# Optimization experiments

Measured on AMD Instinct MI355X. Metric: run time of the kernel, lower is better.

The kernel has to match this reference:

```python
import math
import jax, jax.numpy as jnp
import numpy as np

HIDDEN = 1024
HEADS = 8
HEAD = HIDDEN // HEADS  # 128
BATCH = 512
EPS = 1e-6
GN_EPS = 1e-5


def setup_inputs() -> dict:
    key = jax.random.key(0)
    ks = jax.random.split(key, 12)
    inp = {
        "q": jax.random.normal(ks[0], (BATCH, HIDDEN), jnp.float32),
        "k": jax.random.normal(ks[1], (BATCH, HIDDEN), jnp.float32),
        "v": jax.random.normal(ks[2], (BATCH, HIDDEN), jnp.float32),
        "cell_state": jax.random.normal(ks[3], (BATCH, HEADS, HEAD, HEAD), jnp.float32),
        "norm_state": jax.random.normal(ks[4], (BATCH, HEADS, HEAD), jnp.float32),
        "max_state": jax.random.normal(ks[5], (BATCH, HEADS), jnp.float32),
        # learned params
        "Wi": jax.random.normal(ks[6], (HEADS, 3 * HIDDEN), jnp.float32) / math.sqrt(3 * HIDDEN),
        "bi": jax.random.normal(ks[7], (HEADS,), jnp.float32) * 0.1,
        "Wf": jax.random.normal(ks[8], (HEADS, 3 * HIDDEN), jnp.float32) / math.sqrt(3 * HIDDEN),
        "bf": jax.random.normal(ks[9], (HEADS,), jnp.float32) * 0.1,
        "gn_gamma": jnp.ones((HIDDEN,), jnp.float32),
        "gn_beta": jnp.zeros((HIDDEN,), jnp.float32),
    }
    return inp


def reference(q, k, v, cell_state, norm_state, max_state, Wi, bi, Wf, bf, gn_gamma, gn_beta):
    B, H, D = q.shape[0], HEADS, HEAD
    qkv = jnp.concatenate([q, k, v], axis=-1)           # (B, 3*hidden)
    igate_preact = qkv @ Wi.T + bi                       # (B, H)
    fgate_preact = qkv @ Wf.T + bf                       # (B, H)

    qh = q.reshape(B, H, D)
    kh = k.reshape(B, H, D) * (1.0 / math.sqrt(D))
    vh = v.reshape(B, H, D)

    log_f = jax.nn.log_sigmoid(fgate_preact)
    max_new = jnp.maximum(igate_preact, max_state + log_f)
    i_gate = jnp.exp(igate_preact - max_new)             # (B, H)
    f_gate = jnp.exp(log_f + max_state - max_new)        # (B, H)

    # matrix state update: (B, H, D, D)
    cell_new = f_gate[:, :, None, None] * cell_state + \
               i_gate[:, :, None, None] * kh[:, :, :, None] * vh[:, :, None, :]
    norm_new = f_gate[:, :, None] * norm_state + i_gate[:, :, None] * kh

    numerator = jnp.einsum('bnh,bnhk->bnk', qh, cell_new)   # (B, H, D)
    qn_dot = jnp.einsum('bnh,bnh->bn', qh, norm_new)        # (B, H)
    denominator = jnp.maximum(jnp.abs(qn_dot), jnp.exp(-max_new)) + EPS
    out = numerator / denominator[:, :, None]               # (B, H, D)

    # GroupNorm: num_groups = H, per-group over D channels, per-channel affine
    mu = jnp.mean(out, axis=-1, keepdims=True)
    var = jnp.var(out, axis=-1, keepdims=True)
    out = (out - mu) / jnp.sqrt(var + GN_EPS)
    out = out.reshape(B, H * D) * gn_gamma + gn_beta

    return out, cell_new, norm_new, max_new
```

## Files before the change

### kernel.cpp

```cpp
#include <hip/hip_runtime.h>
#include <math.h>

#define HIDDEN 1024
#define HEADS 8
#define HEAD 128
#define BATCH 512
#define RSQRT_D 0.08838834764831845f

__global__ __launch_bounds__(256) void gates_kernel(
    const float* __restrict__ q, const float* __restrict__ k,
    const float* __restrict__ v, const float* __restrict__ max_state,
    const float* __restrict__ Wi, const float* __restrict__ bi,
    const float* __restrict__ Wf, const float* __restrict__ bf,
    float* __restrict__ ig_out, float* __restrict__ fg_out,
    float* __restrict__ expnm_out, float* __restrict__ maxnew_out)
{
    const int b = blockIdx.x;
    const int t = threadIdx.x;

    float acc_i[HEADS], acc_f[HEADS];
    #pragma unroll
    for (int h = 0; h < HEADS; ++h) { acc_i[h] = 0.f; acc_f[h] = 0.f; }

    const float* qr = q + b * HIDDEN;
    const float* kr = k + b * HIDDEN;
    const float* vr = v + b * HIDDEN;

    for (int j = t; j < 3 * HIDDEN; j += 256) {
        float x = (j < HIDDEN) ? qr[j]
                : (j < 2 * HIDDEN) ? kr[j - HIDDEN]
                : vr[j - 2 * HIDDEN];
        #pragma unroll
        for (int h = 0; h < HEADS; ++h) {
            acc_i[h] = fmaf(x, Wi[h * 3 * HIDDEN + j], acc_i[h]);
            acc_f[h] = fmaf(x, Wf[h * 3 * HIDDEN + j], acc_f[h]);
        }
    }

    #pragma unroll
    for (int h = 0; h < HEADS; ++h) {
        #pragma unroll
        for (int off = 32; off > 0; off >>= 1) {
            acc_i[h] += __shfl_down(acc_i[h], off, 64);
            acc_f[h] += __shfl_down(acc_f[h], off, 64);
        }
    }

    __shared__ float part[4][16];
    __shared__ float pre[16];
    const int wave = t >> 6, lane = t & 63;
    if (lane == 0) {
        #pragma unroll
        for (int h = 0; h < HEADS; ++h) {
            part[wave][h]     = acc_i[h];
            part[wave][8 + h] = acc_f[h];
        }
    }
    __syncthreads();
    if (t < 16) pre[t] = part[0][t] + part[1][t] + part[2][t] + part[3][t];
    __syncthreads();

    if (t < HEADS) {
        float igp = pre[t] + bi[t];
        float fgp = pre[8 + t] + bf[t];
        float lf = (fgp >= 0.f) ? -log1pf(expf(-fgp)) : (fgp - log1pf(expf(fgp)));
        float m_old = max_state[b * HEADS + t];
        float m_new = fmaxf(igp, m_old + lf);
        const int idx = b * HEADS + t;
        ig_out[idx]    = expf(igp - m_new);
        fg_out[idx]    = expf(lf + m_old - m_new);
        expnm_out[idx] = expf(-m_new);
        maxnew_out[idx] = m_new;
    }
}

__global__ __launch_bounds__(256) void mlstm_main(
    const float* __restrict__ q, const float* __restrict__ k,
    const float* __restrict__ v,
    const float* __restrict__ cell_state, const float* __restrict__ norm_state,
    const float* __restrict__ gn_gamma, const float* __restrict__ gn_beta,
    const float* __restrict__ ig, const float* __restrict__ fg,
    const float* __restrict__ expnm,
    float* __restrict__ out, float* __restrict__ cell_new,
    float* __restrict__ norm_new)
{
    const int bh = blockIdx.x;
    const int b = bh >> 3, h = bh & 7;
    const int t = threadIdx.x;
    const int tx = t & 31, ty = t >> 5;

    __shared__ __align__(16) float q_s[HEAD];
    __shared__ __align__(16) float ikh_s[HEAD];
    __shared__ float4 red[8][32];
    __shared__ float inv_denom_s;

    const float i_gate = ig[bh];
    const float f_gate = fg[bh];

    const float* qrow = q + b * HIDDEN + h * HEAD;
    const float* krow = k + b * HIDDEN + h * HEAD;
    const float* vrow = v + b * HIDDEN + h * HEAD;

    if (t < HEAD) {
        q_s[t]   = qrow[t];
        ikh_s[t] = i_gate * krow[t] * RSQRT_D;
    }
    __syncthreads();

    const float4* c_in  = (const float4*)(cell_state + (size_t)bh * HEAD * HEAD);
    float4*       c_out = (float4*)(cell_new   + (size_t)bh * HEAD * HEAD);

    const float4 v4 = ((const float4*)vrow)[tx];

    float4 num = make_float4(0.f, 0.f, 0.f, 0.f);

    #pragma unroll
    for (int i = 0; i < 16; ++i) {
        const int d1 = ty + (i << 3);
        float4 c = c_in[d1 * 32 + tx];
        const float a = ikh_s[d1];
        float4 nc;
        nc.x = fmaf(f_gate, c.x, a * v4.x);
        nc.y = fmaf(f_gate, c.y, a * v4.y);
        nc.z = fmaf(f_gate, c.z, a * v4.z);
        nc.w = fmaf(f_gate, c.w, a * v4.w);
        c_out[d1 * 32 + tx] = nc;
        const float qd = q_s[d1];
        num.x = fmaf(qd, nc.x, num.x);
        num.y = fmaf(qd, nc.y, num.y);
        num.z = fmaf(qd, nc.z, num.z);
        num.w = fmaf(qd, nc.w, num.w);
    }

    red[ty][tx] = num;
    __syncthreads();

    #pragma unroll
    for (int s = 4; s > 0; s >>= 1) {
        if (ty < s) {
            float4 o = red[ty + s][tx];
            float4 m = red[ty][tx];
            m.x += o.x; m.y += o.y; m.z += o.z; m.w += o.w;
            red[ty][tx] = m;
        }
        __syncthreads();
    }

    if (t < 32) {
        const float4 ns  = ((const float4*)(norm_state + (size_t)bh * HEAD))[t];
        const float4 q4  = ((const float4*)q_s)[t];
        const float4 ik4 = ((const float4*)ikh_s)[t];
        float4 nn;
        nn.x = fmaf(f_gate, ns.x, ik4.x);
        nn.y = fmaf(f_gate, ns.y, ik4.y);
        nn.z = fmaf(f_gate, ns.z, ik4.z);
        nn.w = fmaf(f_gate, ns.w, ik4.w);
        ((float4*)(norm_new + (size_t)bh * HEAD))[t] = nn;

        float qn = q4.x * nn.x + q4.y * nn.y + q4.z * nn.z + q4.w * nn.w;
        #pragma unroll
        for (int off = 16; off > 0; off >>= 1)
            qn += __shfl_down(qn, off, 32);
        if (t == 0) {
            const float denom = fmaxf(fabsf(qn), expnm[bh]) + 1e-6f;
            inv_denom_s = 1.0f / denom;
        }
    }
    __syncthreads();

    if (t < 32) {
        const float inv_d = inv_denom_s;
        const float4 numv = red[0][t];
        float4 o;
        o.x = numv.x * inv_d;
        o.y = numv.y * inv_d;
        o.z = numv.z * inv_d;
        o.w = numv.w * inv_d;

        float s  = o.x + o.y + o.z + o.w;
        float ss = o.x * o.x + o.y * o.y + o.z * o.z + o.w * o.w;
        #pragma unroll
        for (int off = 16; off > 0; off >>= 1) {
            s  += __shfl_down(s,  off, 32);
            ss += __shfl_down(ss, off, 32);
        }
        s  = __shfl(s,  0, 32);
        ss = __shfl(ss, 0, 32);

        const float mean = s * (1.f / 128.f);
        const float var  = ss * (1.f / 128.f) - mean * mean;
        const float rstd = rsqrtf(var + 1e-5f);

        const float4 g4 = ((const float4*)(gn_gamma + h * HEAD))[t];
        const float4 b4 = ((const float4*)(gn_beta  + h * HEAD))[t];
        float4 res;
        res.x = fmaf((o.x - mean) * rstd, g4.x, b4.x);
        res.y = fmaf((o.y - mean) * rstd, g4.y, b4.y);
        res.z = fmaf((o.z - mean) * rstd, g4.z, b4.z);
        res.w = fmaf((o.w - mean) * rstd, g4.w, b4.w);
        ((float4*)(out + (size_t)bh * HEAD))[t] = res;
    }
}

extern "C" void kernel_launch(void* const* d_in, const int* in_sizes, int n_in,
                              void* d_out, int out_size, void* d_ws, size_t ws_size,
                              hipStream_t stream)
{
    const float* q          = (const float*)d_in[0];
    const float* k          = (const float*)d_in[1];
    const float* v          = (const float*)d_in[2];
    const float* cell_state = (const float*)d_in[3];
    const float* norm_state = (const float*)d_in[4];
    const float* max_state  = (const float*)d_in[5];
    const float* Wi         = (const float*)d_in[6];
    const float* bi         = (const float*)d_in[7];
    const float* Wf         = (const float*)d_in[8];
    const float* bf         = (const float*)d_in[9];
    const float* gn_gamma   = (const float*)d_in[10];
    const float* gn_beta    = (const float*)d_in[11];

    float* out      = (float*)d_out;
    float* cell_new = out      + (size_t)BATCH * HIDDEN;
    float* norm_new = cell_new + (size_t)BATCH * HEADS * HEAD * HEAD;
    float* max_new  = norm_new + (size_t)BATCH * HEADS * HEAD;

    float* ig    = (float*)d_ws;
    float* fg    = ig + BATCH * HEADS;
    float* expnm = fg + BATCH * HEADS;

    gates_kernel<<<BATCH, 256, 0, stream>>>(
        q, k, v, max_state, Wi, bi, Wf, bf, ig, fg, expnm, max_new);

    mlstm_main<<<BATCH * HEADS, 256, 0, stream>>>(
        q, k, v, cell_state, norm_state, gn_gamma, gn_beta,
        ig, fg, expnm, out, cell_new, norm_new);
}
```

Before: 482.4 us.

## Fuse gate projection into main mLSTM kernel with nontemporal cell-state streaming

Removes the separate gates kernel and computes each head's input and forget gate preactivations inside the per-(batch,head) block using vectorized dot products over the qkv row. This drops one launch and the workspace round trip. The price is that each block re-reads the full qkv row and both weight rows for its head, so the gate work is done redundantly per head. Cell-state loads and stores now use nontemporal hints to stream the large state without polluting cache, and the 8-row reduction is collapsed into a single-warp serial sum.

```diff
diff --git a/kernel.cpp b/kernel.cpp
--- a/kernel.cpp
+++ b/kernel.cpp
@@ -7,82 +7,22 @@
 #define BATCH 512
 #define RSQRT_D 0.08838834764831845f
 
-__global__ __launch_bounds__(256) void gates_kernel(
-    const float* __restrict__ q, const float* __restrict__ k,
-    const float* __restrict__ v, const float* __restrict__ max_state,
-    const float* __restrict__ Wi, const float* __restrict__ bi,
-    const float* __restrict__ Wf, const float* __restrict__ bf,
-    float* __restrict__ ig_out, float* __restrict__ fg_out,
-    float* __restrict__ expnm_out, float* __restrict__ maxnew_out)
-{
-    const int b = blockIdx.x;
-    const int t = threadIdx.x;
+typedef float f4 __attribute__((ext_vector_type(4)));
 
-    float acc_i[HEADS], acc_f[HEADS];
-    #pragma unroll
-    for (int h = 0; h < HEADS; ++h) { acc_i[h] = 0.f; acc_f[h] = 0.f; }
-
-    const float* qr = q + b * HIDDEN;
-    const float* kr = k + b * HIDDEN;
-    const float* vr = v + b * HIDDEN;
-
-    for (int j = t; j < 3 * HIDDEN; j += 256) {
-        float x = (j < HIDDEN) ? qr[j]
-                : (j < 2 * HIDDEN) ? kr[j - HIDDEN]
-                : vr[j - 2 * HIDDEN];
-        #pragma unroll
-        for (int h = 0; h < HEADS; ++h) {
-            acc_i[h] = fmaf(x, Wi[h * 3 * HIDDEN + j], acc_i[h]);
-            acc_f[h] = fmaf(x, Wf[h * 3 * HIDDEN + j], acc_f[h]);
-        }
-    }
-
-    #pragma unroll
-    for (int h = 0; h < HEADS; ++h) {
-        #pragma unroll
-        for (int off = 32; off > 0; off >>= 1) {
-            acc_i[h] += __shfl_down(acc_i[h], off, 64);
-            acc_f[h] += __shfl_down(acc_f[h], off, 64);
-        }
-    }
-
-    __shared__ float part[4][16];
-    __shared__ float pre[16];
-    const int wave = t >> 6, lane = t & 63;
-    if (lane == 0) {
-        #pragma unroll
-        for (int h = 0; h < HEADS; ++h) {
-            part[wave][h]     = acc_i[h];
-            part[wave][8 + h] = acc_f[h];
-        }
-    }
-    __syncthreads();
-    if (t < 16) pre[t] = part[0][t] + part[1][t] + part[2][t] + part[3][t];
-    __syncthreads();
-
-    if (t < HEADS) {
-        float igp = pre[t] + bi[t];
-        float fgp = pre[8 + t] + bf[t];
-        float lf = (fgp >= 0.f) ? -log1pf(expf(-fgp)) : (fgp - log1pf(expf(fgp)));
-        float m_old = max_state[b * HEADS + t];
-        float m_new = fmaxf(igp, m_old + lf);
-        const int idx = b * HEADS + t;
-        ig_out[idx]    = expf(igp - m_new);
-        fg_out[idx]    = expf(lf + m_old - m_new);
-        expnm_out[idx] = expf(-m_new);
-        maxnew_out[idx] = m_new;
-    }
+__device__ __forceinline__ float dot4(f4 a, f4 b) {
+    return a.x * b.x + a.y * b.y + a.z * b.z + a.w * b.w;
 }
 
-__global__ __launch_bounds__(256) void mlstm_main(
+__global__ __launch_bounds__(256) void mlstm_fused(
     const float* __restrict__ q, const float* __restrict__ k,
     const float* __restrict__ v,
     const float* __restrict__ cell_state, const float* __restrict__ norm_state,
+    const float* __restrict__ max_state,
+    const float* __restrict__ Wi, const float* __restrict__ bi,
+    const float* __restrict__ Wf, const float* __restrict__ bf,
     const float* __restrict__ gn_gamma, const float* __restrict__ gn_beta,
-    const float* __restrict__ ig, const float* __restrict__ fg,
-    const float* __restrict__ expnm,
     float* __restrict__ out, float* __restrict__ cell_new,
-    float* __restrict__ norm_new)
+    float* __restrict__ norm_new, float* __restrict__ maxnew_out)
 {
     const int bh = blockIdx.x;
     const int b = bh >> 3, h = bh & 7;
@@ -90,115 +30,121 @@
     const int tx = t & 31, ty = t >> 5;
 
     __shared__ __align__(16) float q_s[HEAD];
-    __shared__ __align__(16) float ikh_s[HEAD];
-    __shared__ float4 red[8][32];
-    __shared__ float inv_denom_s;
-
-    const float i_gate = ig[bh];
-    const float f_gate = fg[bh];
+    __shared__ __align__(16) float kh_s[HEAD];
+    __shared__ f4 red[8][32];
+    __shared__ float part_i[4], part_f[4];
+    __shared__ float gate_s[3];
 
     const float* qrow = q + b * HIDDEN + h * HEAD;
     const float* krow = k + b * HIDDEN + h * HEAD;
     const float* vrow = v + b * HIDDEN + h * HEAD;
 
     if (t < HEAD) {
-        q_s[t]   = qrow[t];
-        ikh_s[t] = i_gate * krow[t] * RSQRT_D;
-    }
-    __syncthreads();
-
-    const float4* c_in  = (const float4*)(cell_state + (size_t)bh * HEAD * HEAD);
-    float4*       c_out = (float4*)(cell_new   + (size_t)bh * HEAD * HEAD);
-
-    const float4 v4 = ((const float4*)vrow)[tx];
-
-    float4 num = make_float4(0.f, 0.f, 0.f, 0.f);
-
-    #pragma unroll
-    for (int i = 0; i < 16; ++i) {
-        const int d1 = ty + (i << 3);
-        float4 c = c_in[d1 * 32 + tx];
-        const float a = ikh_s[d1];
-        float4 nc;
-        nc.x = fmaf(f_gate, c.x, a * v4.x);
-        nc.y = fmaf(f_gate, c.y, a * v4.y);
-        nc.z = fmaf(f_gate, c.z, a * v4.z);
-        nc.w = fmaf(f_gate, c.w, a * v4.w);
-        c_out[d1 * 32 + tx] = nc;
-        const float qd = q_s[d1];
-        num.x = fmaf(qd, nc.x, num.x);
-        num.y = fmaf(qd, nc.y, num.y);
-        num.z = fmaf(qd, nc.z, num.z);
-        num.w = fmaf(qd, nc.w, num.w);
+        q_s[t]  = qrow[t];
+        kh_s[t] = krow[t] * RSQRT_D;
     }
 
-    red[ty][tx] = num;
-    __syncthreads();
+    {
+        const f4* qf = (const f4*)(q + b * HIDDEN);
+        const f4* kf = (const f4*)(k + b * HIDDEN);
+        const f4* vf = (const f4*)(v + b * HIDDEN);
+        const f4* wi = (const f4*)(Wi + h * 3 * HIDDEN);
+        const f4* wf = (const f4*)(Wf + h * 3 * HIDDEN);
 
-    #pragma unroll
-    for (int s = 4; s > 0; s >>= 1) {
-        if (ty < s) {
-            float4 o = red[ty + s][tx];
-            float4 m = red[ty][tx];
-            m.x += o.x; m.y += o.y; m.z += o.z; m.w += o.w;
-            red[ty][tx] = m;
+        const f4 xq = qf[t], xk = kf[t], xv = vf[t];
+        const f4 wiq = wi[t], wik = wi[256 + t], wiv = wi[512 + t];
+        const f4 wfq = wf[t], wfk = wf[256 + t], wfv = wf[512 + t];
+
+        float acc_i = dot4(xq, wiq) + dot4(xk, wik) + dot4(xv, wiv);
+        float acc_f = dot4(xq, wfq) + dot4(xk, wfk) + dot4(xv, wfv);
+
+        #pragma unroll
+        for (int off = 32; off > 0; off >>= 1) {
+            acc_i += __shfl_down(acc_i, off, 64);
+            acc_f += __shfl_down(acc_f, off, 64);
         }
-        __syncthreads();
-    }
-
-    if (t < 32) {
-        const float4 ns  = ((const float4*)(norm_state + (size_t)bh * HEAD))[t];
-        const float4 q4  = ((const float4*)q_s)[t];
-        const float4 ik4 = ((const float4*)ikh_s)[t];
-        float4 nn;
-        nn.x = fmaf(f_gate, ns.x, ik4.x);
-        nn.y = fmaf(f_gate, ns.y, ik4.y);
-        nn.z = fmaf(f_gate, ns.z, ik4.z);
-        nn.w = fmaf(f_gate, ns.w, ik4.w);
-        ((float4*)(norm_new + (size_t)bh * HEAD))[t] = nn;
-
-        float qn = q4.x * nn.x + q4.y * nn.y + q4.z * nn.z + q4.w * nn.w;
-        #pragma unroll
-        for (int off = 16; off > 0; off >>= 1)
-            qn += __shfl_down(qn, off, 32);
-        if (t == 0) {
-            const float denom = fmaxf(fabsf(qn), expnm[bh]) + 1e-6f;
-            inv_denom_s = 1.0f / denom;
+        if ((t & 63) == 0) {
+            part_i[t >> 6] = acc_i;
+            part_f[t >> 6] = acc_f;
         }
     }
     __syncthreads();
 
-    if (t < 32) {
-        const float inv_d = inv_denom_s;
-        const float4 numv = red[0][t];
-        float4 o;
-        o.x = numv.x * inv_d;
-        o.y = numv.y * inv_d;
-        o.z = numv.z * inv_d;
-        o.w = numv.w * inv_d;
+    if (t == 0) {
+        float igp = part_i[0] + part_i[1] + part_i[2] + part_i[3] + bi[h];
+        float fgp = part_f[0] + part_f[1] + part_f[2] + part_f[3] + bf[h];
+        float lf = (fgp >= 0.f) ? -log1pf(expf(-fgp)) : (fgp - log1pf(expf(fgp)));
+        float m_old = max_state[bh];
+        float m_new = fmaxf(igp, m_old + lf);
+        gate_s[0] = expf(igp - m_new);
+        gate_s[1] = expf(lf + m_old - m_new);
+        gate_s[2] = expf(-m_new);
+        maxnew_out[bh] = m_new;
+    }
+    __syncthreads();
 
-        float s  = o.x + o.y + o.z + o.w;
+    const float i_gate = gate_s[0];
+    const float f_gate = gate_s[1];
+
+    const f4* c_in  = (const f4*)(cell_state + (size_t)bh * HEAD * HEAD);
+    f4*       c_out = (f4*)(cell_new + (size_t)bh * HEAD * HEAD);
+    const f4 v4 = ((const f4*)vrow)[tx];
+
+    f4 num = {0.f, 0.f, 0.f, 0.f};
+    #pragma unroll
+    for (int i = 0; i < 16; ++i) {
+        const int d1 = ty + (i << 3);
+        f4 c = __builtin_nontemporal_load(c_in + d1 * 32 + tx);
+        const float a = i_gate * kh_s[d1];
+        f4 nc = f_gate * c + a * v4;
+        __builtin_nontemporal_store(nc, c_out + d1 * 32 + tx);
+        num += q_s[d1] * nc;
+    }
+    red[ty][tx] = num;
+    __syncthreads();
+
+    if (ty == 0) {
+        f4 s = red[0][tx];
+        #pragma unroll
+        for (int r = 1; r < 8; ++r) s += red[r][tx];
+
+        const f4 ns  = ((const f4*)(norm_state + (size_t)bh * HEAD))[tx];
+        const f4 q4  = ((const f4*)q_s)[tx];
+        const f4 kh4 = ((const f4*)kh_s)[tx];
+        f4 nn = f_gate * ns + i_gate * kh4;
+        ((f4*)(norm_new + (size_t)bh * HEAD))[tx] = nn;
+
+        float qn = dot4(q4, nn);
+        #pragma unroll
+        for (int off = 16; off > 0; off >>= 1)
+            qn += __shfl_down(qn, off, 32);
+        qn = __shfl(qn, 0, 32);
+
+        const float inv_d = 1.0f / (fmaxf(fabsf(qn), gate_s[2]) + 1e-6f);
+
+        f4 o = s * inv_d;
+        float sm = o.x + o.y + o.z + o.w;
         float ss = o.x * o.x + o.y * o.y + o.z * o.z + o.w * o.w;
         #pragma unroll
         for (int off = 16; off > 0; off >>= 1) {
-            s  += __shfl_down(s,  off, 32);
+            sm += __shfl_down(sm, off, 32);
             ss += __shfl_down(ss, off, 32);
         }
-        s  = __shfl(s,  0, 32);
+        sm = __shfl(sm, 0, 32);
         ss = __shfl(ss, 0, 32);
 
-        const float mean = s * (1.f / 128.f);
+        const float mean = sm * (1.f / 128.f);
         const float var  = ss * (1.f / 128.f) - mean * mean;
         const float rstd = rsqrtf(var + 1e-5f);
 
-        const float4 g4 = ((const float4*)(gn_gamma + h * HEAD))[t];
-        const float4 b4 = ((const float4*)(gn_beta  + h * HEAD))[t];
-        float4 res;
+        const f4 g4 = ((const f4*)(gn_gamma + h * HEAD))[tx];
+        const f4 b4 = ((const f4*)(gn_beta  + h * HEAD))[tx];
+        f4 res;
         res.x = fmaf((o.x - mean) * rstd, g4.x, b4.x);
         res.y = fmaf((o.y - mean) * rstd, g4.y, b4.y);
         res.z = fmaf((o.z - mean) * rstd, g4.z, b4.z);
         res.w = fmaf((o.w - mean) * rstd, g4.w, b4.w);
-        ((float4*)(out + (size_t)bh * HEAD))[t] = res;
+        ((f4*)(out + (size_t)bh * HEAD))[tx] = res;
     }
 }
 
@@ -224,14 +170,8 @@
     float* norm_new = cell_new + (size_t)BATCH * HEADS * HEAD * HEAD;
     float* max_new  = norm_new + (size_t)BATCH * HEADS * HEAD;
 
-    float* ig    = (float*)d_ws;
-    float* fg    = ig + BATCH * HEADS;
-    float* expnm = fg + BATCH * HEADS;
-
-    gates_kernel<<<BATCH, 256, 0, stream>>>(
-        q, k, v, max_state, Wi, bi, Wf, bf, ig, fg, expnm, max_new);
-
-    mlstm_main<<<BATCH * HEADS, 256, 0, stream>>>(
-        q, k, v, cell_state, norm_state, gn_gamma, gn_beta,
-        ig, fg, expnm, out, cell_new, norm_new);
+    mlstm_fused<<<BATCH * HEADS, 256, 0, stream>>>(
+        q, k, v, cell_state, norm_state, max_state,
+        Wi, bi, Wf, bf, gn_gamma, gn_beta,
+        out, cell_new, norm_new, max_new);
 }
```

Result: faster. 452.2 us (-6.3%).
